# Kernel optimization log

Hardware: AMD Instinct MI355X
Metric: run time of the kernel (lower is better)

The kernel has to match this reference:

```python
import jax, jax.numpy as jnp
import numpy as np

B, H, W, C = 32, 56, 56, 192
WS, SH = 7, 3            # window size, shift size
NH = 6                   # num heads
HD = C // NH             # head dim = 32
N = WS * WS              # tokens per window = 49
NW = (H // WS) * (W // WS)  # windows per image = 64
HID = int(C * 4.0)       # MLP hidden = 768
EPS = 1e-6               # flax LayerNorm default


def _rel_index():
    # (N, N) int index into the (2*WS-1)^2 relative position bias table
    coords = np.stack(np.meshgrid(np.arange(WS), np.arange(WS), indexing='ij')).reshape(2, -1)
    rel = coords[:, :, None] - coords[:, None, :]          # (2, N, N)
    rel = rel.transpose(1, 2, 0) + (WS - 1)                # shift to >= 0
    idx = rel[..., 0] * (2 * WS - 1) + rel[..., 1]
    return jnp.asarray(idx, jnp.int32)


def _attn_mask():
    # standard Swin shifted-window mask: -100 between different regions
    img = np.zeros((H, W))
    cnt = 0
    for hs in (slice(0, -WS), slice(-WS, -SH), slice(-SH, None)):
        for ws in (slice(0, -WS), slice(-WS, -SH), slice(-SH, None)):
            img[hs, ws] = cnt
            cnt += 1
    win = img.reshape(H // WS, WS, W // WS, WS).transpose(0, 2, 1, 3).reshape(NW, N)
    diff = win[:, None, :] - win[:, :, None]
    return jnp.asarray(np.where(diff != 0, -100.0, 0.0), jnp.float32)


def setup_inputs() -> dict:
    key = jax.random.key(0)
    ks = jax.random.split(key, 8)
    s = 0.02
    return {
        'x': jax.random.normal(ks[0], (B, H, W, C), jnp.float32),
        'mask': _attn_mask(),
        'rel_index': _rel_index(),
        'ln1_scale': jnp.ones((C,), jnp.float32),
        'ln1_bias': jnp.zeros((C,), jnp.float32),
        'qkv_w': jax.random.normal(ks[1], (C, 3 * C), jnp.float32) * s,
        'qkv_b': jnp.zeros((3 * C,), jnp.float32),
        'rpb_table': jax.random.normal(ks[2], ((2 * WS - 1) ** 2, NH), jnp.float32) * s,
        'proj_w': jax.random.normal(ks[3], (C, C), jnp.float32) * s,
        'proj_b': jnp.zeros((C,), jnp.float32),
        'ln2_scale': jnp.ones((C,), jnp.float32),
        'ln2_bias': jnp.zeros((C,), jnp.float32),
        'mlp_w1': jax.random.normal(ks[4], (C, HID), jnp.float32) * s,
        'mlp_b1': jnp.zeros((HID,), jnp.float32),
        'mlp_w2': jax.random.normal(ks[5], (HID, C), jnp.float32) * s,
        'mlp_b2': jnp.zeros((C,), jnp.float32),
    }


def _ln(x, scale, bias):
    mu = jnp.mean(x, axis=-1, keepdims=True)
    var = jnp.mean(jnp.square(x - mu), axis=-1, keepdims=True)
    return (x - mu) * jax.lax.rsqrt(var + EPS) * scale + bias


def reference(x, mask, rel_index, ln1_scale, ln1_bias, qkv_w, qkv_b, rpb_table,
              proj_w, proj_b, ln2_scale, ln2_bias, mlp_w1, mlp_b1, mlp_w2, mlp_b2):
    # ---- W-MSA branch ----
    y = _ln(x, ln1_scale, ln1_bias)
    # cyclic shift (grid divisible by window -> pad_to_blocks is a no-op)
    y = jnp.roll(y, shift=(-SH, -SH), axis=(1, 2))
    # window partition: (B,H,W,C) -> (B*NW, N, C)
    y = y.reshape(B, H // WS, WS, W // WS, WS, C).transpose(0, 1, 3, 2, 4, 5)
    y = y.reshape(B * NW, N, C)
    # qkv: (B*NW, N, 3, NH, HD) -> q,k,v each (B*NW, NH, N, HD)
    qkv = (y @ qkv_w + qkv_b).reshape(B * NW, N, 3, NH, HD).transpose(2, 0, 3, 1, 4)
    q, k, v = qkv[0], qkv[1], qkv[2]
    attn = jnp.einsum('bhnd,bhmd->bhnm', q, k) * (HD ** -0.5)
    # relative position bias: (N,N,NH) -> (1,NH,N,N)
    attn = attn + rpb_table[rel_index].transpose(2, 0, 1)[None]
    # shifted-window mask: broadcast over batch and heads
    attn = attn.reshape(B, NW, NH, N, N) + mask[None, :, None]
    attn = jax.nn.softmax(attn.reshape(B * NW, NH, N, N), axis=-1)
    y = jnp.einsum('bhnm,bhmd->bhnd', attn, v).transpose(0, 2, 1, 3).reshape(B * NW, N, C)
    y = y @ proj_w + proj_b
    # window reverse and un-shift
    y = y.reshape(B, H // WS, W // WS, WS, WS, C).transpose(0, 1, 3, 2, 4, 5).reshape(B, H, W, C)
    y = jnp.roll(y, shift=(SH, SH), axis=(1, 2))
    x = x + y
    # ---- MLP branch ----
    z = _ln(x, ln2_scale, ln2_bias)
    z = jax.nn.gelu(z @ mlp_w1 + mlp_b1)  # flax nn.gelu default (tanh approx)
    z = z @ mlp_w2 + mlp_b2
    return x + z
```

## Files before the change

kernel.cpp:

```cpp
#include <hip/hip_runtime.h>


typedef __bf16 bf16_t;
typedef __bf16 bf16x8 __attribute__((ext_vector_type(8)));
typedef float  f32x4  __attribute__((ext_vector_type(4)));

__device__ inline float wred_sum(float v) {
#pragma unroll
  for (int o = 32; o; o >>= 1) v += __shfl_xor(v, o);
  return v;
}

__device__ inline float gelu_tanh(float x) {
  float u = 0.7978845608028654f * (x + 0.044715f * x * x * x);
  float e = __expf(2.f * u);
  float t = 1.f - 2.f / (e + 1.f);
  return 0.5f * x * (1.f + t);
}

__global__ __launch_bounds__(256) void k_ln1_win(
    const float* __restrict__ x, const float* __restrict__ sc,
    const float* __restrict__ bi, bf16_t* __restrict__ yw, int b0, int nTok) {
  int wv = (int)((blockIdx.x * 256 + threadIdx.x) >> 6);
  int lane = threadIdx.x & 63;
  if (wv >= nTok) return;
  int winL = wv / 49;
  int t = wv - winL * 49;
  int wi = winL & 63;
  int b = b0 + (winL >> 6);
  int t7 = t / 7;
  int hr = (wi >> 3) * 7 + t7;
  int wr = (wi & 7) * 7 + (t - t7 * 7);
  int h = hr + 3; if (h >= 56) h -= 56;
  int w = wr + 3; if (w >= 56) w -= 56;
  const float* xp = x + (((size_t)(b * 56 + h)) * 56 + w) * 192;
  float v0 = xp[lane], v1 = xp[lane + 64], v2 = xp[lane + 128];
  float s = wred_sum(v0 + v1 + v2);
  float q = wred_sum(v0 * v0 + v1 * v1 + v2 * v2);
  float mu = s * (1.f / 192.f);
  float var = q * (1.f / 192.f) - mu * mu;
  float rs = rsqrtf(var + 1e-6f);
  bf16_t* op = yw + (size_t)wv * 192;
  op[lane]       = (bf16_t)((v0 - mu) * rs * sc[lane]       + bi[lane]);
  op[lane + 64]  = (bf16_t)((v1 - mu) * rs * sc[lane + 64]  + bi[lane + 64]);
  op[lane + 128] = (bf16_t)((v2 - mu) * rs * sc[lane + 128] + bi[lane + 128]);
}

__global__ __launch_bounds__(256) void k_transpose_cvt(
    const float* __restrict__ in, bf16_t* __restrict__ out, int K, int N) {
  int idx = blockIdx.x * 256 + threadIdx.x;
  if (idx >= K * N) return;
  int n = idx / K, k = idx - n * K;
  out[idx] = (bf16_t)in[(size_t)k * N + n];
}

__global__ __launch_bounds__(128) void k_gemm(
    const bf16_t* __restrict__ A, const bf16_t* __restrict__ Bt,
    const float* __restrict__ bias, void* __restrict__ Cout,
    int M, int Nn, int K, int mode) {
  __shared__ uint4 As[512];
  __shared__ uint4 Bs[256];
  int tid = threadIdx.x;
  int lane = tid & 63, wv = tid >> 6;
  int c = lane & 15, g = lane >> 4;
  int bm = blockIdx.x, bn = blockIdx.y;
  f32x4 acc[4][4] = {};
  const bf16_t* Abase = A + (size_t)bm * 128 * K;
  const bf16_t* Bbase = Bt + (size_t)bn * 64 * K;
  for (int k0 = 0; k0 < K; k0 += 32) {
#pragma unroll
    for (int p = 0; p < 4; ++p) {
      int cid = tid + 128 * p;
      int row = cid >> 2, kg = cid & 3;
      As[row * 4 + (kg ^ ((row >> 1) & 3))] =
          *(const uint4*)(Abase + (size_t)row * K + k0 + kg * 8);
    }
#pragma unroll
    for (int p = 0; p < 2; ++p) {
      int cid = tid + 128 * p;
      int row = cid >> 2, kg = cid & 3;
      Bs[row * 4 + (kg ^ ((row >> 1) & 3))] =
          *(const uint4*)(Bbase + (size_t)row * K + k0 + kg * 8);
    }
    __syncthreads();
    bf16x8 af[4], bfr[4];
#pragma unroll
    for (int i = 0; i < 4; ++i) {
      int ra = wv * 64 + i * 16 + c;
      af[i] = *(const bf16x8*)&As[ra * 4 + (g ^ ((ra >> 1) & 3))];
      int rb = i * 16 + c;
      bfr[i] = *(const bf16x8*)&Bs[rb * 4 + (g ^ ((rb >> 1) & 3))];
    }
#pragma unroll
    for (int i = 0; i < 4; ++i)
#pragma unroll
      for (int j = 0; j < 4; ++j)
        acc[i][j] = __builtin_amdgcn_mfma_f32_16x16x32_bf16(af[i], bfr[j],
                                                            acc[i][j], 0, 0, 0);
    __syncthreads();
  }
#pragma unroll
  for (int j = 0; j < 4; ++j) {
    int col = bn * 64 + j * 16 + c;
    float bv = bias[col];
#pragma unroll
    for (int i = 0; i < 4; ++i) {
#pragma unroll
      for (int r = 0; r < 4; ++r) {
        int row = bm * 128 + wv * 64 + i * 16 + g * 4 + r;
        float v = acc[i][j][r] + bv;
        if (mode == 1) v = gelu_tanh(v);
        if (mode == 2) {
          float* o = (float*)Cout + (size_t)row * Nn + col;
          *o += v;
        } else {
          ((bf16_t*)Cout)[(size_t)row * Nn + col] = (bf16_t)v;
        }
      }
    }
  }
}

__global__ __launch_bounds__(64) void k_attn(
    const bf16_t* __restrict__ qkv, const int* __restrict__ relidx,
    const float* __restrict__ rpb, const float* __restrict__ mask,
    bf16_t* __restrict__ attn_out) {
  __shared__ char sm[8192];
  int blk = blockIdx.x;
  int wL = blk / 6, h = blk - wL * 6;
  int lane = threadIdx.x;
  int c = lane & 15, g = lane >> 4;

  {
    const float* mw = mask + (size_t)(wL & 63) * 2401;
    __bf16* bl = (__bf16*)sm;
    for (int idx = lane; idx < 2401; idx += 64)
      bl[idx] = (__bf16)(rpb[relidx[idx] * 6 + h] + mw[idx]);
  }

  const bf16_t* baseq = qkv + (size_t)wL * (49 * 576);

  f32x4 s[4][4] = {};
  bf16x8 qf[4], kf[4];
#pragma unroll
  for (int i = 0; i < 4; ++i) {
    int n = c + 16 * i; if (n > 48) n = 48;
    qf[i] = *(const bf16x8*)(baseq + (size_t)n * 576 + h * 32 + g * 8);
  }
#pragma unroll
  for (int j = 0; j < 4; ++j) {
    int m = c + 16 * j; if (m > 48) m = 48;
    kf[j] = *(const bf16x8*)(baseq + (size_t)m * 576 + 192 + h * 32 + g * 8);
  }
#pragma unroll
  for (int i = 0; i < 4; ++i)
#pragma unroll
    for (int j = 0; j < 4; ++j)
      s[i][j] = __builtin_amdgcn_mfma_f32_16x16x32_bf16(qf[i], kf[j], s[i][j],
                                                        0, 0, 0);

  const __bf16* bl = (const __bf16*)sm;
  float mxv[4][4], sum[4][4];
#pragma unroll
  for (int i = 0; i < 4; ++i)
#pragma unroll
    for (int r = 0; r < 4; ++r) {
      int n = 16 * i + 4 * g + r;
      int nc = n > 48 ? 48 : n;
      float best = -1e30f;
#pragma unroll
      for (int j = 0; j < 4; ++j) {
        int m = 16 * j + c;
        float v = -1e30f;
        if (m < 49)
          v = s[i][j][r] * 0.17677669529663687f + (float)bl[nc * 49 + m];
        s[i][j][r] = v;
        best = fmaxf(best, v);
      }
      mxv[i][r] = best;
    }
#pragma unroll
  for (int o = 8; o; o >>= 1)
#pragma unroll
    for (int i = 0; i < 4; ++i)
#pragma unroll
      for (int r = 0; r < 4; ++r)
        mxv[i][r] = fmaxf(mxv[i][r], __shfl_xor(mxv[i][r], o));
#pragma unroll
  for (int i = 0; i < 4; ++i)
#pragma unroll
    for (int r = 0; r < 4; ++r) {
      float ss = 0.f;
#pragma unroll
      for (int j = 0; j < 4; ++j) {
        float p = __expf(s[i][j][r] - mxv[i][r]);
        s[i][j][r] = p;
        ss += p;
      }
      sum[i][r] = ss;
    }
#pragma unroll
  for (int o = 8; o; o >>= 1)
#pragma unroll
    for (int i = 0; i < 4; ++i)
#pragma unroll
      for (int r = 0; r < 4; ++r)
        sum[i][r] += __shfl_xor(sum[i][r], o);

#pragma unroll
  for (int i = 0; i < 4; ++i)
#pragma unroll
    for (int j = 0; j < 4; ++j)
#pragma unroll
      for (int r = 0; r < 4; ++r) {
        int n = 16 * i + 4 * g + r;
        int m = 16 * j + c;
        int offb = n * 128 + ((2 * m) ^ ((n & 7) << 4));
        *(__bf16*)(sm + offb) = (__bf16)s[i][j][r];
      }

  f32x4 o2[4][2] = {};
#pragma unroll
  for (int kt = 0; kt < 2; ++kt) {
    bf16x8 pf[4], vf[2];
#pragma unroll
    for (int i = 0; i < 4; ++i) {
      int n = c + 16 * i;
      int cb = (16 * g + 64 * kt) ^ ((n & 7) << 4);
      pf[i] = *(const bf16x8*)(sm + n * 128 + cb);
    }
#pragma unroll
    for (int dt = 0; dt < 2; ++dt) {
      int d = c + 16 * dt;
      union { bf16x8 v; __bf16 e[8]; } u;
#pragma unroll
      for (int e0 = 0; e0 < 8; ++e0) {
        int m = 8 * g + e0 + 32 * kt; if (m > 48) m = 48;
        u.e[e0] = baseq[(size_t)m * 576 + 384 + h * 32 + d];
      }
      vf[dt] = u.v;
    }
#pragma unroll
    for (int i = 0; i < 4; ++i)
#pragma unroll
      for (int dt = 0; dt < 2; ++dt)
        o2[i][dt] = __builtin_amdgcn_mfma_f32_16x16x32_bf16(pf[i], vf[dt],
                                                            o2[i][dt], 0, 0, 0);
  }

#pragma unroll
  for (int i = 0; i < 4; ++i)
#pragma unroll
    for (int dt = 0; dt < 2; ++dt)
#pragma unroll
      for (int r = 0; r < 4; ++r) {
        int n = 16 * i + 4 * g + r;
        if (n < 49) {
          int d = 16 * dt + c;
          attn_out[((size_t)wL * 49 + n) * 192 + h * 32 + d] =
              (bf16_t)(o2[i][dt][r] / sum[i][r]);
        }
      }
}

__global__ __launch_bounds__(256) void k_unwin_ln2(
    const float* __restrict__ x, const bf16_t* __restrict__ projw,
    const float* __restrict__ sc, const float* __restrict__ bi,
    float* __restrict__ out, bf16_t* __restrict__ z, int b0, int nTok) {
  int wv = (int)((blockIdx.x * 256 + threadIdx.x) >> 6);
  int lane = threadIdx.x & 63;
  if (wv >= nTok) return;
  int bL = wv / 3136;
  int rem = wv - bL * 3136;
  int hh = rem / 56, ww2 = rem - hh * 56;
  int b = b0 + bL;
  int hr = hh + 53; if (hr >= 56) hr -= 56;
  int wr = ww2 + 53; if (wr >= 56) wr -= 56;
  int winL = bL * 64 + (hr / 7) * 8 + (wr / 7);
  int t = (hr % 7) * 7 + (wr % 7);
  const bf16_t* pp = projw + ((size_t)winL * 49 + t) * 192;
  size_t gtok = ((size_t)(b * 56 + hh)) * 56 + ww2;
  const float* xp = x + gtok * 192;
  float v0 = xp[lane]       + (float)pp[lane];
  float v1 = xp[lane + 64]  + (float)pp[lane + 64];
  float v2 = xp[lane + 128] + (float)pp[lane + 128];
  float* op = out + gtok * 192;
  op[lane] = v0; op[lane + 64] = v1; op[lane + 128] = v2;
  float s = wred_sum(v0 + v1 + v2);
  float q = wred_sum(v0 * v0 + v1 * v1 + v2 * v2);
  float mu = s * (1.f / 192.f);
  float var = q * (1.f / 192.f) - mu * mu;
  float rs = rsqrtf(var + 1e-6f);
  bf16_t* zp = z + gtok * 192;
  zp[lane]       = (bf16_t)((v0 - mu) * rs * sc[lane]       + bi[lane]);
  zp[lane + 64]  = (bf16_t)((v1 - mu) * rs * sc[lane + 64]  + bi[lane + 64]);
  zp[lane + 128] = (bf16_t)((v2 - mu) * rs * sc[lane + 128] + bi[lane + 128]);
}

extern "C" void kernel_launch(void* const* d_in, const int* in_sizes, int n_in,
                              void* d_out, int out_size, void* d_ws,
                              size_t ws_size, hipStream_t stream) {
  (void)in_sizes; (void)n_in; (void)out_size;
  const float* x     = (const float*)d_in[0];
  const float* maskp = (const float*)d_in[1];
  const int*   reli  = (const int*)d_in[2];
  const float* ln1s  = (const float*)d_in[3];
  const float* ln1b  = (const float*)d_in[4];
  const float* qkvw  = (const float*)d_in[5];
  const float* qkvb  = (const float*)d_in[6];
  const float* rpb   = (const float*)d_in[7];
  const float* projw = (const float*)d_in[8];
  const float* projb = (const float*)d_in[9];
  const float* ln2s  = (const float*)d_in[10];
  const float* ln2b  = (const float*)d_in[11];
  const float* w1    = (const float*)d_in[12];
  const float* b1    = (const float*)d_in[13];
  const float* w2    = (const float*)d_in[14];
  const float* b2    = (const float*)d_in[15];
  float* out = (float*)d_out;

  auto aup = [](size_t v) { return (v + 255) & ~(size_t)255; };
  char* base = (char*)d_ws;
  size_t off = 0;
  bf16_t* z_buf = (bf16_t*)(base + off); off += aup((size_t)100352 * 192 * 2);
  bf16_t* qkvT  = (bf16_t*)(base + off); off += aup((size_t)576 * 192 * 2);
  bf16_t* projT = (bf16_t*)(base + off); off += aup((size_t)192 * 192 * 2);
  bf16_t* w1T   = (bf16_t*)(base + off); off += aup((size_t)768 * 192 * 2);
  bf16_t* w2T   = (bf16_t*)(base + off); off += aup((size_t)192 * 768 * 2);
  size_t offB = off;

  int Bc = 32;
  while (Bc > 2 && offB + (size_t)Bc * 3136 * (576 + 192) * 2 > ws_size)
    Bc >>= 1;
  bf16_t* bufB = (bf16_t*)(base + offB);
  bf16_t* bufA = (bf16_t*)(base + offB + aup((size_t)Bc * 3136 * 576 * 2));

  size_t hBytes = (ws_size > offB) ? (ws_size - offB) : 0;
  long long HcL = (long long)((hBytes / 1536) & ~(size_t)127);
  int Hc = (int)(HcL > 100352 ? 100352 : HcL);
  if (Hc < 128) Hc = 128;

  k_transpose_cvt<<<(192 * 576 + 255) / 256, 256, 0, stream>>>(qkvw, qkvT, 192, 576);
  k_transpose_cvt<<<(192 * 192 + 255) / 256, 256, 0, stream>>>(projw, projT, 192, 192);
  k_transpose_cvt<<<(192 * 768 + 255) / 256, 256, 0, stream>>>(w1, w1T, 192, 768);
  k_transpose_cvt<<<(768 * 192 + 255) / 256, 256, 0, stream>>>(w2, w2T, 768, 192);

  for (int b0 = 0; b0 < 32; b0 += Bc) {
    int nTok = Bc * 3136, nWin = Bc * 64;
    k_ln1_win<<<nTok / 4, 256, 0, stream>>>(x, ln1s, ln1b, bufA, b0, nTok);
    k_gemm<<<dim3(nTok / 128, 576 / 64), 128, 0, stream>>>(
        bufA, qkvT, qkvb, (void*)bufB, nTok, 576, 192, 0);
    k_attn<<<nWin * 6, 64, 0, stream>>>(bufB, reli, rpb, maskp, bufA);
    k_gemm<<<dim3(nTok / 128, 192 / 64), 128, 0, stream>>>(
        bufA, projT, projb, (void*)bufB, nTok, 192, 192, 0);
    k_unwin_ln2<<<nTok / 4, 256, 0, stream>>>(x, bufB, ln2s, ln2b, out, z_buf,
                                              b0, nTok);
  }

  for (int r0 = 0; r0 < 100352; r0 += Hc) {
    int rows = 100352 - r0; if (rows > Hc) rows = Hc;
    k_gemm<<<dim3(rows / 128, 768 / 64), 128, 0, stream>>>(
        z_buf + (size_t)r0 * 192, w1T, b1, (void*)bufB, rows, 768, 192, 1);
    k_gemm<<<dim3(rows / 128, 192 / 64), 128, 0, stream>>>(
        bufB, w2T, b2, (void*)(out + (size_t)r0 * 192), rows, 192, 768, 2);
  }
}
```

Measured before the change: 697.8 us.

## Fuse MLP GEMMs through LDS and use register-resident weight persistent GEMM

```diff
diff --git a/kernel.cpp b/kernel.cpp
--- a/kernel.cpp
+++ b/kernel.cpp
@@ -54,68 +54,53 @@
   out[idx] = (bf16_t)in[(size_t)k * N + n];
 }
 
-__global__ __launch_bounds__(128) void k_gemm(
+template <int K>
+__global__ __launch_bounds__(256, 2) void k_gemm_bs(
     const bf16_t* __restrict__ A, const bf16_t* __restrict__ Bt,
-    const float* __restrict__ bias, void* __restrict__ Cout,
-    int M, int Nn, int K, int mode) {
-  __shared__ uint4 As[512];
-  __shared__ uint4 Bs[256];
+    const float* __restrict__ bias, bf16_t* __restrict__ C, int Nn, int nMt) {
+  constexpr int NKS = K / 32;
   int tid = threadIdx.x;
-  int lane = tid & 63, wv = tid >> 6;
+  int w = tid >> 6, lane = tid & 63;
   int c = lane & 15, g = lane >> 4;
-  int bm = blockIdx.x, bn = blockIdx.y;
-  f32x4 acc[4][4] = {};
-  const bf16_t* Abase = A + (size_t)bm * 128 * K;
-  const bf16_t* Bbase = Bt + (size_t)bn * 64 * K;
-  for (int k0 = 0; k0 < K; k0 += 32) {
-#pragma unroll
-    for (int p = 0; p < 4; ++p) {
-      int cid = tid + 128 * p;
-      int row = cid >> 2, kg = cid & 3;
-      As[row * 4 + (kg ^ ((row >> 1) & 3))] =
-          *(const uint4*)(Abase + (size_t)row * K + k0 + kg * 8);
-    }
-#pragma unroll
-    for (int p = 0; p < 2; ++p) {
-      int cid = tid + 128 * p;
-      int row = cid >> 2, kg = cid & 3;
-      Bs[row * 4 + (kg ^ ((row >> 1) & 3))] =
-          *(const uint4*)(Bbase + (size_t)row * K + k0 + kg * 8);
-    }
-    __syncthreads();
-    bf16x8 af[4], bfr[4];
-#pragma unroll
-    for (int i = 0; i < 4; ++i) {
-      int ra = wv * 64 + i * 16 + c;
-      af[i] = *(const bf16x8*)&As[ra * 4 + (g ^ ((ra >> 1) & 3))];
-      int rb = i * 16 + c;
-      bfr[i] = *(const bf16x8*)&Bs[rb * 4 + (g ^ ((rb >> 1) & 3))];
-    }
-#pragma unroll
-    for (int i = 0; i < 4; ++i)
-#pragma unroll
-      for (int j = 0; j < 4; ++j)
-        acc[i][j] = __builtin_amdgcn_mfma_f32_16x16x32_bf16(af[i], bfr[j],
-                                                            acc[i][j], 0, 0, 0);
-    __syncthreads();
-  }
-#pragma unroll
-  for (int j = 0; j < 4; ++j) {
-    int col = bn * 64 + j * 16 + c;
-    float bv = bias[col];
-#pragma unroll
-    for (int i = 0; i < 4; ++i) {
-#pragma unroll
-      for (int r = 0; r < 4; ++r) {
-        int row = bm * 128 + wv * 64 + i * 16 + g * 4 + r;
-        float v = acc[i][j][r] + bv;
-        if (mode == 1) v = gelu_tanh(v);
-        if (mode == 2) {
-          float* o = (float*)Cout + (size_t)row * Nn + col;
-          *o += v;
-        } else {
-          ((bf16_t*)Cout)[(size_t)row * Nn + col] = (bf16_t)v;
-        }
+  int bn = blockIdx.x;
+  bf16x8 bf[4][NKS];
+  const bf16_t* bp = Bt + (size_t)(bn * 64 + c) * K + 8 * g;
+#pragma unroll
+  for (int jc = 0; jc < 4; ++jc)
+#pragma unroll
+    for (int ks = 0; ks < NKS; ++ks)
+      bf[jc][ks] = *(const bf16x8*)(bp + (size_t)jc * 16 * K + 32 * ks);
+  float4 bias4[4];
+#pragma unroll
+  for (int jc = 0; jc < 4; ++jc)
+    bias4[jc] = *(const float4*)(bias + bn * 64 + jc * 16 + 4 * g);
+  for (int mt = blockIdx.y; mt < nMt; mt += gridDim.y) {
+    int m0 = mt * 256 + w * 64;
+    f32x4 acc[4][4] = {};
+    const bf16_t* ap = A + (size_t)(m0 + c) * K + 8 * g;
+#pragma unroll
+    for (int ks = 0; ks < NKS; ++ks) {
+      bf16x8 af[4];
+#pragma unroll
+      for (int ir = 0; ir < 4; ++ir)
+        af[ir] = *(const bf16x8*)(ap + (size_t)ir * 16 * K + 32 * ks);
+#pragma unroll
+      for (int jc = 0; jc < 4; ++jc)
+#pragma unroll
+        for (int ir = 0; ir < 4; ++ir)
+          acc[jc][ir] = __builtin_amdgcn_mfma_f32_16x16x32_bf16(
+              bf[jc][ks], af[ir], acc[jc][ir], 0, 0, 0);
+    }
+#pragma unroll
+    for (int ir = 0; ir < 4; ++ir) {
+      bf16_t* cp = C + (size_t)(m0 + ir * 16 + c) * Nn + bn * 64 + 4 * g;
+#pragma unroll
+      for (int jc = 0; jc < 4; ++jc) {
+        union { uint2 u; bf16_t e[4]; } pk;
+#pragma unroll
+        for (int r = 0; r < 4; ++r)
+          pk.e[r] = (bf16_t)(acc[jc][ir][r] + ((const float*)&bias4[jc])[r]);
+        *(uint2*)(cp + jc * 16) = pk.u;
       }
     }
   }
@@ -130,16 +115,13 @@
   int wL = blk / 6, h = blk - wL * 6;
   int lane = threadIdx.x;
   int c = lane & 15, g = lane >> 4;
-
   {
     const float* mw = mask + (size_t)(wL & 63) * 2401;
     __bf16* bl = (__bf16*)sm;
     for (int idx = lane; idx < 2401; idx += 64)
       bl[idx] = (__bf16)(rpb[relidx[idx] * 6 + h] + mw[idx]);
   }
-
   const bf16_t* baseq = qkv + (size_t)wL * (49 * 576);
-
   f32x4 s[4][4] = {};
   bf16x8 qf[4], kf[4];
 #pragma unroll
@@ -158,7 +140,6 @@
     for (int j = 0; j < 4; ++j)
       s[i][j] = __builtin_amdgcn_mfma_f32_16x16x32_bf16(qf[i], kf[j], s[i][j],
                                                         0, 0, 0);
-
   const __bf16* bl = (const __bf16*)sm;
   float mxv[4][4], sum[4][4];
 #pragma unroll
@@ -206,7 +187,6 @@
 #pragma unroll
       for (int r = 0; r < 4; ++r)
         sum[i][r] += __shfl_xor(sum[i][r], o);
-
 #pragma unroll
   for (int i = 0; i < 4; ++i)
 #pragma unroll
@@ -218,7 +198,6 @@
         int offb = n * 128 + ((2 * m) ^ ((n & 7) << 4));
         *(__bf16*)(sm + offb) = (__bf16)s[i][j][r];
       }
-
   f32x4 o2[4][2] = {};
 #pragma unroll
   for (int kt = 0; kt < 2; ++kt) {
@@ -247,7 +226,6 @@
         o2[i][dt] = __builtin_amdgcn_mfma_f32_16x16x32_bf16(pf[i], vf[dt],
                                                             o2[i][dt], 0, 0, 0);
   }
-
 #pragma unroll
   for (int i = 0; i < 4; ++i)
 #pragma unroll
@@ -297,6 +275,90 @@
   zp[lane + 128] = (bf16_t)((v2 - mu) * rs * sc[lane + 128] + bi[lane + 128]);
 }
 
+__global__ __launch_bounds__(256, 2) void k_mlp_fused(
+    const bf16_t* __restrict__ z, const bf16_t* __restrict__ w1T,
+    const float* __restrict__ b1, const bf16_t* __restrict__ w2T,
+    const float* __restrict__ b2, float* __restrict__ out) {
+  __shared__ char hsm[128 * 256];
+  int tid = threadIdx.x;
+  int w = tid >> 6, lane = tid & 63;
+  int c = lane & 15, g = lane >> 4;
+  int wr = w >> 1, wc = w & 1;
+  int m0 = blockIdx.x * 128;
+  f32x4 acc2[6][4] = {};
+  for (int hc = 0; hc < 6; ++hc) {
+    f32x4 acc1[4][4] = {};
+    const bf16_t* zp = z + (size_t)(m0 + wr * 64 + c) * 192 + 8 * g;
+    const bf16_t* w1p = w1T + (size_t)(hc * 128 + wc * 64 + c) * 192 + 8 * g;
+#pragma unroll
+    for (int ks = 0; ks < 6; ++ks) {
+      bf16x8 zf[4], wf[4];
+#pragma unroll
+      for (int i = 0; i < 4; ++i) {
+        zf[i] = *(const bf16x8*)(zp + (size_t)i * 16 * 192 + 32 * ks);
+        wf[i] = *(const bf16x8*)(w1p + (size_t)i * 16 * 192 + 32 * ks);
+      }
+#pragma unroll
+      for (int jh = 0; jh < 4; ++jh)
+#pragma unroll
+        for (int ir = 0; ir < 4; ++ir)
+          acc1[jh][ir] = __builtin_amdgcn_mfma_f32_16x16x32_bf16(
+              wf[jh], zf[ir], acc1[jh][ir], 0, 0, 0);
+    }
+    if (hc) __syncthreads();
+#pragma unroll
+    for (int jh = 0; jh < 4; ++jh) {
+      float4 b1v = *(const float4*)(b1 + hc * 128 + wc * 64 + jh * 16 + 4 * g);
+#pragma unroll
+      for (int ir = 0; ir < 4; ++ir) {
+        union { uint2 u; __bf16 e[4]; } pk;
+#pragma unroll
+        for (int r = 0; r < 4; ++r)
+          pk.e[r] = (__bf16)gelu_tanh(acc1[jh][ir][r] + ((const float*)&b1v)[r]);
+        int row = wr * 64 + ir * 16 + c;
+        int byo = (wc * 64 + jh * 16 + 4 * g) * 2;
+        *(uint2*)(hsm + row * 256 + (byo ^ ((row & 7) << 4))) = pk.u;
+      }
+    }
+    __syncthreads();
+    const bf16_t* w2p = w2T + (size_t)(wc * 96 + c) * 768 + hc * 128 + 8 * g;
+#pragma unroll
+    for (int ks = 0; ks < 4; ++ks) {
+      bf16x8 hf[4], wf2[6];
+#pragma unroll
+      for (int ir = 0; ir < 4; ++ir) {
+        int row = wr * 64 + ir * 16 + c;
+        int byo = 16 * g + 64 * ks;
+        hf[ir] = *(const bf16x8*)(hsm + row * 256 + (byo ^ ((row & 7) << 4)));
+      }
+#pragma unroll
+      for (int jc = 0; jc < 6; ++jc)
+        wf2[jc] = *(const bf16x8*)(w2p + (size_t)jc * 16 * 768 + 32 * ks);
+#pragma unroll
+      for (int jc = 0; jc < 6; ++jc)
+#pragma unroll
+        for (int ir = 0; ir < 4; ++ir)
+          acc2[jc][ir] = __builtin_amdgcn_mfma_f32_16x16x32_bf16(
+              wf2[jc], hf[ir], acc2[jc][ir], 0, 0, 0);
+    }
+  }
+#pragma unroll
+  for (int jc = 0; jc < 6; ++jc) {
+    float4 b2v = *(const float4*)(b2 + wc * 96 + jc * 16 + 4 * g);
+#pragma unroll
+    for (int ir = 0; ir < 4; ++ir) {
+      int row = m0 + wr * 64 + ir * 16 + c;
+      float* op = out + (size_t)row * 192 + wc * 96 + jc * 16 + 4 * g;
+      float4 cur = *(float4*)op;
+      cur.x += acc2[jc][ir][0] + b2v.x;
+      cur.y += acc2[jc][ir][1] + b2v.y;
+      cur.z += acc2[jc][ir][2] + b2v.z;
+      cur.w += acc2[jc][ir][3] + b2v.w;
+      *(float4*)op = cur;
+    }
+  }
+}
+
 extern "C" void kernel_launch(void* const* d_in, const int* in_sizes, int n_in,
                               void* d_out, int out_size, void* d_ws,
                               size_t ws_size, hipStream_t stream) {
@@ -330,15 +392,10 @@
   size_t offB = off;
 
   int Bc = 32;
-  while (Bc > 2 && offB + (size_t)Bc * 3136 * (576 + 192) * 2 > ws_size)
+  while (Bc > 4 && offB + (size_t)Bc * 3136 * (576 + 192) * 2 > ws_size)
     Bc >>= 1;
   bf16_t* bufB = (bf16_t*)(base + offB);
   bf16_t* bufA = (bf16_t*)(base + offB + aup((size_t)Bc * 3136 * 576 * 2));
-
-  size_t hBytes = (ws_size > offB) ? (ws_size - offB) : 0;
-  long long HcL = (long long)((hBytes / 1536) & ~(size_t)127);
-  int Hc = (int)(HcL > 100352 ? 100352 : HcL);
-  if (Hc < 128) Hc = 128;
 
   k_transpose_cvt<<<(192 * 576 + 255) / 256, 256, 0, stream>>>(qkvw, qkvT, 192, 576);
   k_transpose_cvt<<<(192 * 192 + 255) / 256, 256, 0, stream>>>(projw, projT, 192, 192);
@@ -347,21 +404,24 @@
 
   for (int b0 = 0; b0 < 32; b0 += Bc) {
     int nTok = Bc * 3136, nWin = Bc * 64;
+    int nMt = nTok / 256;
     k_ln1_win<<<nTok / 4, 256, 0, stream>>>(x, ln1s, ln1b, bufA, b0, nTok);
-    k_gemm<<<dim3(nTok / 128, 576 / 64), 128, 0, stream>>>(
-        bufA, qkvT, qkvb, (void*)bufB, nTok, 576, 192, 0);
+    {
+      int nbn = 576 / 64;
+      int gy = (512 + nbn - 1) / nbn; if (gy > nMt) gy = nMt;
+      k_gemm_bs<192><<<dim3(nbn, gy), 256, 0, stream>>>(bufA, qkvT, qkvb, bufB,
+                                                        576, nMt);
+    }
     k_attn<<<nWin * 6, 64, 0, stream>>>(bufB, reli, rpb, maskp, bufA);
-    k_gemm<<<dim3(nTok / 128, 192 / 64), 128, 0, stream>>>(
-        bufA, projT, projb, (void*)bufB, nTok, 192, 192, 0);
+    {
+      int nbn = 192 / 64;
+      int gy = (512 + nbn - 1) / nbn; if (gy > nMt) gy = nMt;
+      k_gemm_bs<192><<<dim3(nbn, gy), 256, 0, stream>>>(bufA, projT, projb,
+                                                        bufB, 192, nMt);
+    }
     k_unwin_ln2<<<nTok / 4, 256, 0, stream>>>(x, bufB, ln2s, ln2b, out, z_buf,
                                               b0, nTok);
   }
 
-  for (int r0 = 0; r0 < 100352; r0 += Hc) {
-    int rows = 100352 - r0; if (rows > Hc) rows = Hc;
-    k_gemm<<<dim3(rows / 128, 768 / 64), 128, 0, stream>>>(
-        z_buf + (size_t)r0 * 192, w1T, b1, (void*)bufB, rows, 768, 192, 1);
-    k_gemm<<<dim3(rows / 128, 192 / 64), 128, 0, stream>>>(
-        bufB, w2T, b2, (void*)(out + (size_t)r0 * 192), rows, 192, 768, 2);
-  }
-}
+  k_mlp_fused<<<100352 / 128, 256, 0, stream>>>(z_buf, w1T, b1, w2T, b2, out);
+}
```

Measured after the change: 678.6 us. 1.03x faster.
